# Kernel optimization log

Hardware: AMD Instinct MI355X
Metric: run time of the kernel (lower is better)

## Reference

```python
import jax, jax.numpy as jnp
import numpy as np

H = 128

def _rnn_layer(inp, W_ih, W_hh, b_ih, b_hh):
    # inp: [B, T, D]; precompute the input projection for all timesteps at once
    pre = jnp.einsum('btd,hd->bth', inp, W_ih) + b_ih + b_hh  # [B, T, H]
    B = inp.shape[0]
    h0 = jnp.zeros((B, H), dtype=inp.dtype)

    def step(h, p_t):  # p_t: [B, H]
        h_new = jnp.tanh(p_t + h @ W_hh.T)
        return h_new, h_new

    _, hs = jax.lax.scan(step, h0, jnp.swapaxes(pre, 0, 1))  # [T, B, H]
    return jnp.swapaxes(hs, 0, 1)  # [B, T, H]


def setup_inputs() -> dict:
    key = jax.random.key(0)
    ks = jax.random.split(key, 12)
    B, T, D = 64, 512, 2048
    s_in = 1.0 / np.sqrt(H)  # PyTorch RNN init scale ~ U(-1/sqrt(H), 1/sqrt(H))
    u = lambda k, shape: jax.random.uniform(k, shape, jnp.float32, -s_in, s_in)
    return {
        'x': jax.random.normal(ks[0], (B, T, D), jnp.float32),
        'W_ih1': u(ks[1], (H, D)),
        'W_hh1': u(ks[2], (H, H)),
        'b_ih1': u(ks[3], (H,)),
        'b_hh1': u(ks[4], (H,)),
        'W_ih2': u(ks[5], (H, H)),
        'W_hh2': u(ks[6], (H, H)),
        'b_ih2': u(ks[7], (H,)),
        'b_hh2': u(ks[8], (H,)),
        'W_fc': u(ks[9], (1, H)),
        'b_fc': u(ks[10], (1,)),
    }


def reference(x, W_ih1, W_hh1, b_ih1, b_hh1, W_ih2, W_hh2, b_ih2, b_hh2, W_fc, b_fc):
    h1 = _rnn_layer(x, W_ih1, W_hh1, b_ih1, b_hh1)   # [B, T, H]
    h2 = _rnn_layer(h1, W_ih2, W_hh2, b_ih2, b_hh2)  # [B, T, H]
    last = h2[:, -1, :]                               # [B, H]
    return last @ W_fc.T + b_fc                       # [B, 1]
```

## Files before the change

kernel.cpp:

```cpp
#include <hip/hip_runtime.h>
#include <cstddef>

#define BB 64
#define TT 512
#define DD 2048
#define HH 128
#define M1 (BB*TT)

__device__ __forceinline__ float tanh_fast(float x) {
    float e2x = __builtin_amdgcn_exp2f(x * 2.885390081777927f);
    return 1.0f - 2.0f * __builtin_amdgcn_rcpf(e2x + 1.0f);
}

template<int K>
__global__ __launch_bounds__(256) void gemm_bias_kernel(
    const float* __restrict__ A, const float* __restrict__ W,
    const float* __restrict__ bia, const float* __restrict__ bib,
    float* __restrict__ out)
{
    constexpr int BM = 64, BK = 16;
    constexpr int NK = K / BK;
    __shared__ float As[BK][68];
    __shared__ float Bs[BK][132];

    const int tid = threadIdx.x;
    const int tc = tid & 15;
    const int tr = tid >> 4;
    const size_t m0 = (size_t)blockIdx.x * BM;

    const int arow = tid >> 2;
    const int ak4  = (tid & 3) * 4;
    const int bn0  = tid >> 1;
    const int bk   = (tid & 1) * 8;

    const float* Aptr = A + (m0 + arow) * (size_t)K + ak4;
    const float* Wptr = W + (size_t)bn0 * K + bk;

    float4 ra  = *(const float4*)Aptr;
    float4 rb0 = *(const float4*)(Wptr);
    float4 rb1 = *(const float4*)(Wptr + 4);

    float acc[4][8];
#pragma unroll
    for (int i = 0; i < 4; i++)
#pragma unroll
        for (int j = 0; j < 8; j++) acc[i][j] = 0.0f;

    for (int kt = 0; kt < NK; ++kt) {
        __syncthreads();
        As[ak4 + 0][arow] = ra.x;
        As[ak4 + 1][arow] = ra.y;
        As[ak4 + 2][arow] = ra.z;
        As[ak4 + 3][arow] = ra.w;
        Bs[bk + 0][bn0] = rb0.x;
        Bs[bk + 1][bn0] = rb0.y;
        Bs[bk + 2][bn0] = rb0.z;
        Bs[bk + 3][bn0] = rb0.w;
        Bs[bk + 4][bn0] = rb1.x;
        Bs[bk + 5][bn0] = rb1.y;
        Bs[bk + 6][bn0] = rb1.z;
        Bs[bk + 7][bn0] = rb1.w;
        __syncthreads();
        if (kt + 1 < NK) {
            ra  = *(const float4*)(Aptr + (size_t)(kt + 1) * BK);
            rb0 = *(const float4*)(Wptr + (size_t)(kt + 1) * BK);
            rb1 = *(const float4*)(Wptr + (size_t)(kt + 1) * BK + 4);
        }
#pragma unroll
        for (int kk = 0; kk < BK; ++kk) {
            const float4 av = *(const float4*)&As[kk][tr * 4];
            const float4 b0 = *(const float4*)&Bs[kk][tc * 4];
            const float4 b1 = *(const float4*)&Bs[kk][64 + tc * 4];
            const float aa[4] = {av.x, av.y, av.z, av.w};
            const float bb[8] = {b0.x, b0.y, b0.z, b0.w, b1.x, b1.y, b1.z, b1.w};
#pragma unroll
            for (int i = 0; i < 4; i++)
#pragma unroll
                for (int j = 0; j < 8; j++)
                    acc[i][j] = __builtin_fmaf(aa[i], bb[j], acc[i][j]);
        }
    }

    float bs[8];
#pragma unroll
    for (int j = 0; j < 4; j++) {
        bs[j]     = bia[tc * 4 + j] + bib[tc * 4 + j];
        bs[j + 4] = bia[64 + tc * 4 + j] + bib[64 + tc * 4 + j];
    }
#pragma unroll
    for (int i = 0; i < 4; i++) {
        const size_t r = m0 + tr * 4 + i;
        float4 o0 = {acc[i][0] + bs[0], acc[i][1] + bs[1],
                     acc[i][2] + bs[2], acc[i][3] + bs[3]};
        float4 o1 = {acc[i][4] + bs[4], acc[i][5] + bs[5],
                     acc[i][6] + bs[6], acc[i][7] + bs[7]};
        *(float4*)&out[r * HH + tc * 4]      = o0;
        *(float4*)&out[r * HH + 64 + tc * 4] = o1;
    }
}

__global__ __launch_bounds__(512) void rnn_scan_kernel(
    const float* __restrict__ pre,
    const float* __restrict__ Whh,
    float* __restrict__ hout,
    const float* __restrict__ Wfc,
    const float* __restrict__ bfc,
    float* __restrict__ outv,
    const int store_h)
{
    __shared__ float hsh[2][160];
    __shared__ float wsum[8];

    const int tid  = threadIdx.x;
    const int wave = tid >> 6;
    const int lane = tid & 63;
    const int jj   = lane >> 3;
    const int kq   = lane & 7;
    const int j    = wave * 8 + jj;
    const int b    = blockIdx.x;


    float4 Wr0[4], Wr1[4];
    {
        const float* wp0 = Whh + (size_t)j * HH + kq * 16;
        const float* wp1 = Whh + (size_t)(j + 64) * HH + kq * 16;
#pragma unroll
        for (int q = 0; q < 4; q++) {
            Wr0[q] = *(const float4*)(wp0 + q * 4);
            Wr1[q] = *(const float4*)(wp1 + q * 4);
        }
    }

    if (tid < HH) hsh[0][(tid >> 4) * 20 + (tid & 15)] = 0.0f;
    __syncthreads();

    const float* pb = pre + (size_t)b * TT * HH;
    float pre_next0 = 0.f, pre_next1 = 0.f;
    if (kq == 0) { pre_next0 = pb[j]; pre_next1 = pb[j + 64]; }
    float hlast0 = 0.f, hlast1 = 0.f;

    for (int t = 0; t < TT; ++t) {
        const float* hr = hsh[t & 1];
        float* hw = hsh[(t + 1) & 1];
        const float pre_cur0 = pre_next0, pre_cur1 = pre_next1;
        if (kq == 0 && t + 1 < TT) {
            pre_next0 = pb[(size_t)(t + 1) * HH + j];
            pre_next1 = pb[(size_t)(t + 1) * HH + j + 64];
        }
        float acc0 = 0.f, acc1 = 0.f;
#pragma unroll
        for (int q = 0; q < 4; q++) {
            const float4 hv = *(const float4*)&hr[kq * 20 + q * 4];
            acc0 = __builtin_fmaf(Wr0[q].x, hv.x, acc0);
            acc0 = __builtin_fmaf(Wr0[q].y, hv.y, acc0);
            acc0 = __builtin_fmaf(Wr0[q].z, hv.z, acc0);
            acc0 = __builtin_fmaf(Wr0[q].w, hv.w, acc0);
            acc1 = __builtin_fmaf(Wr1[q].x, hv.x, acc1);
            acc1 = __builtin_fmaf(Wr1[q].y, hv.y, acc1);
            acc1 = __builtin_fmaf(Wr1[q].z, hv.z, acc1);
            acc1 = __builtin_fmaf(Wr1[q].w, hv.w, acc1);
        }
        acc0 += __shfl_xor(acc0, 1);  acc1 += __shfl_xor(acc1, 1);
        acc0 += __shfl_xor(acc0, 2);  acc1 += __shfl_xor(acc1, 2);
        acc0 += __shfl_xor(acc0, 4);  acc1 += __shfl_xor(acc1, 4);
        if (kq == 0) {
            const float h0 = tanh_fast(pre_cur0 + acc0);
            const float h1 = tanh_fast(pre_cur1 + acc1);
            hw[(j >> 4) * 20 + (j & 15)] = h0;
            hw[((j + 64) >> 4) * 20 + ((j + 64) & 15)] = h1;
            if (store_h) {
                hout[((size_t)b * TT + t) * HH + j]      = h0;
                hout[((size_t)b * TT + t) * HH + j + 64] = h1;
            }
            hlast0 = h0; hlast1 = h1;
        }
        __syncthreads();
    }

    if (!store_h) {
        float contrib = 0.f;
        if (kq == 0) contrib = hlast0 * Wfc[j] + hlast1 * Wfc[j + 64];
#pragma unroll
        for (int off = 1; off < 64; off <<= 1) contrib += __shfl_xor(contrib, off);
        if (lane == 0) wsum[wave] = contrib;
        __syncthreads();
        if (tid == 0) {
            float s = bfc[0];
#pragma unroll
            for (int w = 0; w < 8; w++) s += wsum[w];
            outv[b] = s;
        }
    }
}

extern "C" void kernel_launch(void* const* d_in, const int* in_sizes, int n_in,
                              void* d_out, int out_size, void* d_ws, size_t ws_size,
                              hipStream_t stream) {
    const float* x    = (const float*)d_in[0];
    const float* Wih1 = (const float*)d_in[1];
    const float* Whh1 = (const float*)d_in[2];
    const float* bih1 = (const float*)d_in[3];
    const float* bhh1 = (const float*)d_in[4];
    const float* Wih2 = (const float*)d_in[5];
    const float* Whh2 = (const float*)d_in[6];
    const float* bih2 = (const float*)d_in[7];
    const float* bhh2 = (const float*)d_in[8];
    const float* Wfc  = (const float*)d_in[9];
    const float* bfc  = (const float*)d_in[10];
    float* out = (float*)d_out;

    float* preA = (float*)d_ws;
    float* h1b  = preA + (size_t)M1 * HH;

    gemm_bias_kernel<DD><<<dim3(M1 / 64), dim3(256), 0, stream>>>(x, Wih1, bih1, bhh1, preA);
    rnn_scan_kernel<<<dim3(BB), dim3(512), 0, stream>>>(preA, Whh1, h1b, Wfc, bfc, out, 1);
    gemm_bias_kernel<HH><<<dim3(M1 / 64), dim3(256), 0, stream>>>(h1b, Wih2, bih2, bhh2, preA);
    rnn_scan_kernel<<<dim3(BB), dim3(512), 0, stream>>>(preA, Whh2, h1b, Wfc, bfc, out, 0);
}
```

Baseline: 940.5 us.

## Use split-bf16 MFMA for input GEMM and single-wave f16 dot2 RNN scan

The first input-projection GEMM now runs on matrix cores. Activations and weights are split into hi/lo bf16 parts and combined with three MFMAs per tile to keep near-fp32 accuracy; a small prep kernel splits the weights first. The recurrent scan moves to one 64-lane wave per batch row. It keeps W_hh in registers as packed fp16, uses fdot2, and drops the block-wide barriers and shuffle reductions of the 512-thread version. In exchange the recurrence runs in fp16, which loses precision, and the scan depends on in-wave LDS ordering with no explicit barrier.

Measured after the change: 938.6 us. Within noise of the previous version (-0.2%).

```diff
diff --git a/kernel.cpp b/kernel.cpp
--- a/kernel.cpp
+++ b/kernel.cpp
@@ -1,5 +1,6 @@
 #include <hip/hip_runtime.h>
 #include <cstddef>
+#include <cstdint>
 
 #define BB 64
 #define TT 512
@@ -7,9 +8,112 @@
 #define HH 128
 #define M1 (BB*TT)
 
+typedef __attribute__((ext_vector_type(8))) short bf16x8;
+typedef __attribute__((ext_vector_type(4))) float f32x4;
+typedef __attribute__((ext_vector_type(2))) _Float16 h2f;
+
+__device__ __forceinline__ unsigned short f2bf(float f) {
+    unsigned u = __builtin_bit_cast(unsigned, f);
+    u += 0x7fffu + ((u >> 16) & 1u);
+    return (unsigned short)(u >> 16);
+}
+__device__ __forceinline__ float bf2f(unsigned short s) {
+    return __builtin_bit_cast(float, ((unsigned)s) << 16);
+}
 __device__ __forceinline__ float tanh_fast(float x) {
     float e2x = __builtin_amdgcn_exp2f(x * 2.885390081777927f);
     return 1.0f - 2.0f * __builtin_amdgcn_rcpf(e2x + 1.0f);
+}
+
+__global__ __launch_bounds__(256) void prep_w_kernel(
+    const float* __restrict__ W,
+    unsigned short* __restrict__ Whi, unsigned short* __restrict__ Wlo)
+{
+    const int i = (blockIdx.x * 256 + threadIdx.x) * 4;
+    float4 w = *(const float4*)(W + i);
+    unsigned short h0 = f2bf(w.x), h1 = f2bf(w.y), h2 = f2bf(w.z), h3 = f2bf(w.w);
+    unsigned short l0 = f2bf(w.x - bf2f(h0)), l1 = f2bf(w.y - bf2f(h1));
+    unsigned short l2 = f2bf(w.z - bf2f(h2)), l3 = f2bf(w.w - bf2f(h3));
+    ushort4 hv; hv.x = h0; hv.y = h1; hv.z = h2; hv.w = h3;
+    ushort4 lv; lv.x = l0; lv.y = l1; lv.z = l2; lv.w = l3;
+    *(ushort4*)(Whi + i) = hv;
+    *(ushort4*)(Wlo + i) = lv;
+}
+
+__global__ __launch_bounds__(256) void gemm1_mfma_kernel(
+    const float* __restrict__ A, const unsigned short* __restrict__ Whi,
+    const unsigned short* __restrict__ Wlo,
+    const float* __restrict__ bia, const float* __restrict__ bib,
+    float* __restrict__ out)
+{
+    constexpr int K = DD, BK = 32, NK = K / BK;
+    __shared__ __align__(16) short Ah[64 * 40];
+    __shared__ __align__(16) short Al[64 * 40];
+    __shared__ __align__(16) short Wh[128 * 40];
+    __shared__ __align__(16) short Wl[128 * 40];
+
+    const int tid = threadIdx.x, wave = tid >> 6, lane = tid & 63;
+    const size_t m0 = (size_t)blockIdx.x * 64;
+    const int ar = tid >> 2, ak = (tid & 3) * 8;
+    const int wr = tid >> 1, wk = (tid & 1) * 16;
+    const float* Ap = A + (m0 + ar) * (size_t)K + ak;
+    const unsigned short* Whp = Whi + (size_t)wr * K + wk;
+    const unsigned short* Wlp = Wlo + (size_t)wr * K + wk;
+    const int frow = lane & 15, fko = (lane >> 4) * 8;
+
+    f32x4 acc[8];
+#pragma unroll
+    for (int i = 0; i < 8; i++) acc[i] = (f32x4){0.f, 0.f, 0.f, 0.f};
+
+    for (int kt = 0; kt < NK; ++kt) {
+        float4 a0 = *(const float4*)(Ap + kt * BK);
+        float4 a1 = *(const float4*)(Ap + kt * BK + 4);
+        bf16x8 wh0 = *(const bf16x8*)(Whp + kt * BK);
+        bf16x8 wh1 = *(const bf16x8*)(Whp + kt * BK + 8);
+        bf16x8 wl0 = *(const bf16x8*)(Wlp + kt * BK);
+        bf16x8 wl1 = *(const bf16x8*)(Wlp + kt * BK + 8);
+        __syncthreads();
+        float fv[8] = {a0.x, a0.y, a0.z, a0.w, a1.x, a1.y, a1.z, a1.w};
+        unsigned short h[8], l[8];
+#pragma unroll
+        for (int i = 0; i < 8; i++) {
+            h[i] = f2bf(fv[i]);
+            l[i] = f2bf(fv[i] - bf2f(h[i]));
+        }
+        uint2 p0, p1, q0, q1;
+        p0.x = (unsigned)h[0] | ((unsigned)h[1] << 16); p0.y = (unsigned)h[2] | ((unsigned)h[3] << 16);
+        p1.x = (unsigned)h[4] | ((unsigned)h[5] << 16); p1.y = (unsigned)h[6] | ((unsigned)h[7] << 16);
+        q0.x = (unsigned)l[0] | ((unsigned)l[1] << 16); q0.y = (unsigned)l[2] | ((unsigned)l[3] << 16);
+        q1.x = (unsigned)l[4] | ((unsigned)l[5] << 16); q1.y = (unsigned)l[6] | ((unsigned)l[7] << 16);
+        *(uint2*)&Ah[ar * 40 + ak]     = p0;
+        *(uint2*)&Ah[ar * 40 + ak + 4] = p1;
+        *(uint2*)&Al[ar * 40 + ak]     = q0;
+        *(uint2*)&Al[ar * 40 + ak + 4] = q1;
+        *(bf16x8*)&Wh[wr * 40 + wk]     = wh0;
+        *(bf16x8*)&Wh[wr * 40 + wk + 8] = wh1;
+        *(bf16x8*)&Wl[wr * 40 + wk]     = wl0;
+        *(bf16x8*)&Wl[wr * 40 + wk + 8] = wl1;
+        __syncthreads();
+        bf16x8 fAh = *(const bf16x8*)&Ah[(wave * 16 + frow) * 40 + fko];
+        bf16x8 fAl = *(const bf16x8*)&Al[(wave * 16 + frow) * 40 + fko];
+#pragma unroll
+        for (int nt = 0; nt < 8; ++nt) {
+            bf16x8 fWh = *(const bf16x8*)&Wh[(nt * 16 + frow) * 40 + fko];
+            bf16x8 fWl = *(const bf16x8*)&Wl[(nt * 16 + frow) * 40 + fko];
+            acc[nt] = __builtin_amdgcn_mfma_f32_16x16x32_bf16(fAh, fWh, acc[nt], 0, 0, 0);
+            acc[nt] = __builtin_amdgcn_mfma_f32_16x16x32_bf16(fAh, fWl, acc[nt], 0, 0, 0);
+            acc[nt] = __builtin_amdgcn_mfma_f32_16x16x32_bf16(fAl, fWh, acc[nt], 0, 0, 0);
+        }
+    }
+    const int rbase = (lane >> 4) * 4;
+#pragma unroll
+    for (int nt = 0; nt < 8; ++nt) {
+        const int col = nt * 16 + frow;
+        const float bv = bia[col] + bib[col];
+#pragma unroll
+        for (int r = 0; r < 4; r++)
+            out[(m0 + wave * 16 + rbase + r) * HH + col] = acc[nt][r] + bv;
+    }
 }
 
 template<int K>
@@ -22,47 +126,32 @@
     constexpr int NK = K / BK;
     __shared__ float As[BK][68];
     __shared__ float Bs[BK][132];
-
     const int tid = threadIdx.x;
-    const int tc = tid & 15;
-    const int tr = tid >> 4;
+    const int tc = tid & 15, tr = tid >> 4;
     const size_t m0 = (size_t)blockIdx.x * BM;
-
-    const int arow = tid >> 2;
-    const int ak4  = (tid & 3) * 4;
-    const int bn0  = tid >> 1;
-    const int bk   = (tid & 1) * 8;
-
+    const int arow = tid >> 2, ak4 = (tid & 3) * 4;
+    const int bn0 = tid >> 1, bk = (tid & 1) * 8;
     const float* Aptr = A + (m0 + arow) * (size_t)K + ak4;
     const float* Wptr = W + (size_t)bn0 * K + bk;
-
-    float4 ra  = *(const float4*)Aptr;
+    float4 ra = *(const float4*)Aptr;
     float4 rb0 = *(const float4*)(Wptr);
     float4 rb1 = *(const float4*)(Wptr + 4);
-
     float acc[4][8];
 #pragma unroll
     for (int i = 0; i < 4; i++)
 #pragma unroll
         for (int j = 0; j < 8; j++) acc[i][j] = 0.0f;
-
     for (int kt = 0; kt < NK; ++kt) {
         __syncthreads();
-        As[ak4 + 0][arow] = ra.x;
-        As[ak4 + 1][arow] = ra.y;
-        As[ak4 + 2][arow] = ra.z;
-        As[ak4 + 3][arow] = ra.w;
-        Bs[bk + 0][bn0] = rb0.x;
-        Bs[bk + 1][bn0] = rb0.y;
-        Bs[bk + 2][bn0] = rb0.z;
-        Bs[bk + 3][bn0] = rb0.w;
-        Bs[bk + 4][bn0] = rb1.x;
-        Bs[bk + 5][bn0] = rb1.y;
-        Bs[bk + 6][bn0] = rb1.z;
-        Bs[bk + 7][bn0] = rb1.w;
+        As[ak4 + 0][arow] = ra.x; As[ak4 + 1][arow] = ra.y;
+        As[ak4 + 2][arow] = ra.z; As[ak4 + 3][arow] = ra.w;
+        Bs[bk + 0][bn0] = rb0.x; Bs[bk + 1][bn0] = rb0.y;
+        Bs[bk + 2][bn0] = rb0.z; Bs[bk + 3][bn0] = rb0.w;
+        Bs[bk + 4][bn0] = rb1.x; Bs[bk + 5][bn0] = rb1.y;
+        Bs[bk + 6][bn0] = rb1.z; Bs[bk + 7][bn0] = rb1.w;
         __syncthreads();
         if (kt + 1 < NK) {
-            ra  = *(const float4*)(Aptr + (size_t)(kt + 1) * BK);
+            ra = *(const float4*)(Aptr + (size_t)(kt + 1) * BK);
             rb0 = *(const float4*)(Wptr + (size_t)(kt + 1) * BK);
             rb1 = *(const float4*)(Wptr + (size_t)(kt + 1) * BK + 4);
         }
@@ -80,116 +169,94 @@
                     acc[i][j] = __builtin_fmaf(aa[i], bb[j], acc[i][j]);
         }
     }
-
     float bs[8];
 #pragma unroll
     for (int j = 0; j < 4; j++) {
-        bs[j]     = bia[tc * 4 + j] + bib[tc * 4 + j];
+        bs[j] = bia[tc * 4 + j] + bib[tc * 4 + j];
         bs[j + 4] = bia[64 + tc * 4 + j] + bib[64 + tc * 4 + j];
     }
 #pragma unroll
     for (int i = 0; i < 4; i++) {
         const size_t r = m0 + tr * 4 + i;
-        float4 o0 = {acc[i][0] + bs[0], acc[i][1] + bs[1],
-                     acc[i][2] + bs[2], acc[i][3] + bs[3]};
-        float4 o1 = {acc[i][4] + bs[4], acc[i][5] + bs[5],
-                     acc[i][6] + bs[6], acc[i][7] + bs[7]};
-        *(float4*)&out[r * HH + tc * 4]      = o0;
+        float4 o0 = {acc[i][0] + bs[0], acc[i][1] + bs[1], acc[i][2] + bs[2], acc[i][3] + bs[3]};
+        float4 o1 = {acc[i][4] + bs[4], acc[i][5] + bs[5], acc[i][6] + bs[6], acc[i][7] + bs[7]};
+        *(float4*)&out[r * HH + tc * 4] = o0;
         *(float4*)&out[r * HH + 64 + tc * 4] = o1;
     }
 }
 
-__global__ __launch_bounds__(512) void rnn_scan_kernel(
+__global__ __launch_bounds__(64) void rnn_scan_f16(
     const float* __restrict__ pre,
     const float* __restrict__ Whh,
     float* __restrict__ hout,
-    const float* __restrict__ Wfc,
-    const float* __restrict__ bfc,
+    const float* __restrict__ Wfc, const float* __restrict__ bfc,
     float* __restrict__ outv,
     const int store_h)
 {
-    __shared__ float hsh[2][160];
-    __shared__ float wsum[8];
-
-    const int tid  = threadIdx.x;
-    const int wave = tid >> 6;
-    const int lane = tid & 63;
-    const int jj   = lane >> 3;
-    const int kq   = lane & 7;
-    const int j    = wave * 8 + jj;
-    const int b    = blockIdx.x;
-
-
-    float4 Wr0[4], Wr1[4];
+    __shared__ __align__(16) _Float16 hsf[HH];
+    const int l = threadIdx.x;
+    const int b = blockIdx.x;
+
+    h2f W0[64], W1[64];
     {
-        const float* wp0 = Whh + (size_t)j * HH + kq * 16;
-        const float* wp1 = Whh + (size_t)(j + 64) * HH + kq * 16;
-#pragma unroll
-        for (int q = 0; q < 4; q++) {
-            Wr0[q] = *(const float4*)(wp0 + q * 4);
-            Wr1[q] = *(const float4*)(wp1 + q * 4);
-        }
-    }
-
-    if (tid < HH) hsh[0][(tid >> 4) * 20 + (tid & 15)] = 0.0f;
-    __syncthreads();
+        const float* r0 = Whh + l * HH;
+        const float* r1 = Whh + (l + 64) * HH;
+#pragma unroll
+        for (int q = 0; q < 32; q++) {
+            float4 w = *(const float4*)(r0 + q * 4);
+            W0[2 * q]     = h2f{(_Float16)w.x, (_Float16)w.y};
+            W0[2 * q + 1] = h2f{(_Float16)w.z, (_Float16)w.w};
+            float4 v = *(const float4*)(r1 + q * 4);
+            W1[2 * q]     = h2f{(_Float16)v.x, (_Float16)v.y};
+            W1[2 * q + 1] = h2f{(_Float16)v.z, (_Float16)v.w};
+        }
+    }
+    hsf[l] = (_Float16)0.f;
+    hsf[l + 64] = (_Float16)0.f;
 
     const float* pb = pre + (size_t)b * TT * HH;
-    float pre_next0 = 0.f, pre_next1 = 0.f;
-    if (kq == 0) { pre_next0 = pb[j]; pre_next1 = pb[j + 64]; }
-    float hlast0 = 0.f, hlast1 = 0.f;
+    float* hob = hout + (size_t)b * TT * HH;
+    float pn0 = pb[l], pn1 = pb[l + 64];
+    float fc0 = 0.f;
 
     for (int t = 0; t < TT; ++t) {
-        const float* hr = hsh[t & 1];
-        float* hw = hsh[(t + 1) & 1];
-        const float pre_cur0 = pre_next0, pre_cur1 = pre_next1;
-        if (kq == 0 && t + 1 < TT) {
-            pre_next0 = pb[(size_t)(t + 1) * HH + j];
-            pre_next1 = pb[(size_t)(t + 1) * HH + j + 64];
-        }
-        float acc0 = 0.f, acc1 = 0.f;
-#pragma unroll
-        for (int q = 0; q < 4; q++) {
-            const float4 hv = *(const float4*)&hr[kq * 20 + q * 4];
-            acc0 = __builtin_fmaf(Wr0[q].x, hv.x, acc0);
-            acc0 = __builtin_fmaf(Wr0[q].y, hv.y, acc0);
-            acc0 = __builtin_fmaf(Wr0[q].z, hv.z, acc0);
-            acc0 = __builtin_fmaf(Wr0[q].w, hv.w, acc0);
-            acc1 = __builtin_fmaf(Wr1[q].x, hv.x, acc1);
-            acc1 = __builtin_fmaf(Wr1[q].y, hv.y, acc1);
-            acc1 = __builtin_fmaf(Wr1[q].z, hv.z, acc1);
-            acc1 = __builtin_fmaf(Wr1[q].w, hv.w, acc1);
-        }
-        acc0 += __shfl_xor(acc0, 1);  acc1 += __shfl_xor(acc1, 1);
-        acc0 += __shfl_xor(acc0, 2);  acc1 += __shfl_xor(acc1, 2);
-        acc0 += __shfl_xor(acc0, 4);  acc1 += __shfl_xor(acc1, 4);
-        if (kq == 0) {
-            const float h0 = tanh_fast(pre_cur0 + acc0);
-            const float h1 = tanh_fast(pre_cur1 + acc1);
-            hw[(j >> 4) * 20 + (j & 15)] = h0;
-            hw[((j + 64) >> 4) * 20 + ((j + 64) & 15)] = h1;
-            if (store_h) {
-                hout[((size_t)b * TT + t) * HH + j]      = h0;
-                hout[((size_t)b * TT + t) * HH + j + 64] = h1;
-            }
-            hlast0 = h0; hlast1 = h1;
-        }
-        __syncthreads();
+        const float p0 = pn0, p1 = pn1;
+        if (t + 1 < TT) {
+            pn0 = pb[(size_t)(t + 1) * HH + l];
+            pn1 = pb[(size_t)(t + 1) * HH + l + 64];
+        }
+        float a0 = 0.f, a0b = 0.f, a1 = 0.f, a1b = 0.f;
+#pragma unroll
+        for (int q = 0; q < 16; q++) {
+            uint4 hv = *(const uint4*)&hsf[q * 8];
+            h2f x0 = __builtin_bit_cast(h2f, hv.x);
+            h2f x1 = __builtin_bit_cast(h2f, hv.y);
+            h2f x2 = __builtin_bit_cast(h2f, hv.z);
+            h2f x3 = __builtin_bit_cast(h2f, hv.w);
+            a0  = __builtin_amdgcn_fdot2(W0[4 * q],     x0, a0,  false);
+            a0b = __builtin_amdgcn_fdot2(W0[4 * q + 1], x1, a0b, false);
+            a0  = __builtin_amdgcn_fdot2(W0[4 * q + 2], x2, a0,  false);
+            a0b = __builtin_amdgcn_fdot2(W0[4 * q + 3], x3, a0b, false);
+            a1  = __builtin_amdgcn_fdot2(W1[4 * q],     x0, a1,  false);
+            a1b = __builtin_amdgcn_fdot2(W1[4 * q + 1], x1, a1b, false);
+            a1  = __builtin_amdgcn_fdot2(W1[4 * q + 2], x2, a1,  false);
+            a1b = __builtin_amdgcn_fdot2(W1[4 * q + 3], x3, a1b, false);
+        }
+        const float h0 = tanh_fast(p0 + a0 + a0b);
+        const float h1 = tanh_fast(p1 + a1 + a1b);
+        hsf[l] = (_Float16)h0;
+        hsf[l + 64] = (_Float16)h1;
+        if (store_h) {
+            hob[(size_t)t * HH + l] = h0;
+            hob[(size_t)t * HH + l + 64] = h1;
+        }
+        if (t == TT - 1) fc0 = h0 * Wfc[l] + h1 * Wfc[l + 64];
     }
 
     if (!store_h) {
-        float contrib = 0.f;
-        if (kq == 0) contrib = hlast0 * Wfc[j] + hlast1 * Wfc[j + 64];
-#pragma unroll
-        for (int off = 1; off < 64; off <<= 1) contrib += __shfl_xor(contrib, off);
-        if (lane == 0) wsum[wave] = contrib;
-        __syncthreads();
-        if (tid == 0) {
-            float s = bfc[0];
-#pragma unroll
-            for (int w = 0; w < 8; w++) s += wsum[w];
-            outv[b] = s;
-        }
+#pragma unroll
+        for (int off = 1; off < 64; off <<= 1) fc0 += __shfl_xor(fc0, off);
+        if (l == 0) outv[b] = fc0 + bfc[0];
     }
 }
 
@@ -211,9 +278,12 @@
 
     float* preA = (float*)d_ws;
     float* h1b  = preA + (size_t)M1 * HH;
-
-    gemm_bias_kernel<DD><<<dim3(M1 / 64), dim3(256), 0, stream>>>(x, Wih1, bih1, bhh1, preA);
-    rnn_scan_kernel<<<dim3(BB), dim3(512), 0, stream>>>(preA, Whh1, h1b, Wfc, bfc, out, 1);
+    unsigned short* Whi = (unsigned short*)h1b;
+    unsigned short* Wlo = Whi + (size_t)HH * DD;
+
+    prep_w_kernel<<<dim3(HH * DD / 1024), dim3(256), 0, stream>>>(Wih1, Whi, Wlo);
+    gemm1_mfma_kernel<<<dim3(M1 / 64), dim3(256), 0, stream>>>(x, Whi, Wlo, bih1, bhh1, preA);
+    rnn_scan_f16<<<dim3(BB), dim3(64), 0, stream>>>(preA, Whh1, h1b, Wfc, bfc, out, 1);
     gemm_bias_kernel<HH><<<dim3(M1 / 64), dim3(256), 0, stream>>>(h1b, Wih2, bih2, bhh2, preA);
-    rnn_scan_kernel<<<dim3(BB), dim3(512), 0, stream>>>(preA, Whh2, h1b, Wfc, bfc, out, 0);
-}
+    rnn_scan_f16<<<dim3(BB), dim3(64), 0, stream>>>(preA, Whh2, h1b, Wfc, bfc, out, 0);
+}
```
